# Kernel optimization log

Measured on AMD Instinct MI355X. Metric: run time of the kernel, lower is better.

Reference implementation:

```python
import math
import jax, jax.numpy as jnp
import numpy as np

B, S, D, H = 2, 2048, 1024, 16
DK = D // H


def alibi_slopes(n_heads):
    # canonical ALiBi slopes for power-of-two head counts: 2^(-8*(h+1)/H)
    ratio = 2.0 ** (-8.0 / n_heads)
    return jnp.asarray(ratio ** np.arange(1, n_heads + 1), dtype=jnp.float32)


def setup_inputs() -> dict:
    key = jax.random.key(0)
    ks = jax.random.split(key, 8)
    std = 1.0 / math.sqrt(D)
    return {
        "query": jax.random.normal(ks[0], (B, S, D), jnp.float32),
        "key": jax.random.normal(ks[1], (B, S, D), jnp.float32),
        "value": jax.random.normal(ks[2], (B, S, D), jnp.float32),
        "mask": jnp.ones((B, S, S), jnp.int32),
        "Wq": jax.random.normal(ks[3], (D, D), jnp.float32) * std,
        "bq": jnp.zeros((D,), jnp.float32),
        "Wk": jax.random.normal(ks[4], (D, D), jnp.float32) * std,
        "bk": jnp.zeros((D,), jnp.float32),
        "Wv": jax.random.normal(ks[5], (D, D), jnp.float32) * std,
        "bv": jnp.zeros((D,), jnp.float32),
        "Wo": jax.random.normal(ks[6], (D, D), jnp.float32) * std,
        "bo": jnp.zeros((D,), jnp.float32),
    }


def _split_heads(x):
    # [B, S, D] -> [B, H, S, DK]
    return x.reshape(B, -1, H, DK).transpose(0, 2, 1, 3)


def reference(query, key, value, mask, Wq, bq, Wk, bk, Wv, bv, Wo, bo):
    q = _split_heads(query @ Wq + bq)
    k = _split_heads(key @ Wk + bk)
    v = _split_heads(value @ Wv + bv)
    scores = jnp.einsum("bhqd,bhkd->bhqk", q, k) / math.sqrt(DK)
    # ALiBi bias: -slope_h * |i - j|, shape [H, S, S]
    pos = jnp.arange(S)
    dist = jnp.abs(pos[:, None] - pos[None, :]).astype(jnp.float32)
    bias = -alibi_slopes(H)[:, None, None] * dist
    scores = scores + bias[None]
    scores = jnp.where(mask[:, None] == 0, -jnp.inf, scores)
    p_attn = jax.nn.softmax(scores, axis=-1)
    out = jnp.einsum("bhqk,bhkd->bhqd", p_attn, v)
    out = out.transpose(0, 2, 1, 3).reshape(B, -1, D)
    return out @ Wo + bo
```

## Files before the change

kernel.cpp:

```cpp
#include <hip/hip_runtime.h>
#include <hip/hip_bf16.h>
#include <math.h>

constexpr int Bb  = 2;
constexpr int Ss  = 2048;
constexpr int Dd  = 1024;
constexpr int Hh  = 16;
constexpr int DKk = 64;
constexpr int Mm  = Bb * Ss;

#define QSCALE 0.18033688f

typedef unsigned short u16;
typedef unsigned int   u32;
typedef __attribute__((ext_vector_type(8))) short short8;
typedef __attribute__((ext_vector_type(4))) short short4v;
typedef __attribute__((ext_vector_type(4))) float f32x4;
typedef __attribute__((ext_vector_type(4))) int   int4v;

static __device__ __forceinline__ u16 f2bf(float f) {
  union { float f; unsigned u; } c; c.f = f;
  unsigned u = c.u;
  unsigned r = u + 0x7FFFu + ((u >> 16) & 1u);
  return (u16)(r >> 16);
}

static __device__ __forceinline__ void gl_lds16(const u16* g, u16* l) {
  __builtin_amdgcn_global_load_lds(
      (const __attribute__((address_space(1))) u32*)g,
      (__attribute__((address_space(3))) u32*)l, 16, 0, 0);
}

__global__ __launch_bounds__(256) void cvt_inputs(
    const float* __restrict__ q, const float* __restrict__ k,
    const float* __restrict__ v, u16* __restrict__ outA)
{
  const size_t per = (size_t)Mm * Dd / 4;
  const size_t tot = 3 * per;
  for (size_t i = (size_t)blockIdx.x * blockDim.x + threadIdx.x; i < tot;
       i += (size_t)gridDim.x * blockDim.x) {
    const float* src; size_t idx;
    if (i < per)            { src = q; idx = i; }
    else if (i < 2 * per)   { src = k; idx = i - per; }
    else                    { src = v; idx = i - 2 * per; }
    f32x4 f = ((const f32x4*)src)[idx];
    short4v o;
    o[0] = (short)f2bf(f[0]); o[1] = (short)f2bf(f[1]);
    o[2] = (short)f2bf(f[2]); o[3] = (short)f2bf(f[3]);
    ((short4v*)outA)[i] = o;
  }
}

__global__ __launch_bounds__(256) void wt_transpose(
    const float* __restrict__ wq, const float* __restrict__ wk,
    const float* __restrict__ wv, const float* __restrict__ wo,
    u16* __restrict__ outWT)
{
  __shared__ float tile[64][65];
  const int z = blockIdx.z;
  const float* w = (z == 0) ? wq : (z == 1) ? wk : (z == 2) ? wv : wo;
  const int n0 = blockIdx.x * 64, k0 = blockIdx.y * 64;
  const int t = threadIdx.x;
  {
    const int r = t >> 2, u = t & 3;
    #pragma unroll
    for (int e = 0; e < 4; e++) {
      f32x4 f = *(const f32x4*)(w + (size_t)(k0 + r) * Dd + n0 + u * 16 + e * 4);
      tile[r][u * 16 + e * 4 + 0] = f[0];
      tile[r][u * 16 + e * 4 + 1] = f[1];
      tile[r][u * 16 + e * 4 + 2] = f[2];
      tile[r][u * 16 + e * 4 + 3] = f[3];
    }
  }
  __syncthreads();
  {
    const int n = t >> 2, u = t & 3;
    u16 tmp[16];
    #pragma unroll
    for (int e = 0; e < 16; e++) tmp[e] = f2bf(tile[u * 16 + e][n]);
    short8 o0, o1;
    #pragma unroll
    for (int j = 0; j < 8; j++) { o0[j] = (short)tmp[j]; o1[j] = (short)tmp[8 + j]; }
    u16* dst = outWT + (size_t)z * Dd * Dd + (size_t)(n0 + n) * Dd + k0 + u * 16;
    *(short8*)dst       = o0;
    *(short8*)(dst + 8) = o1;
  }
}

__global__ __launch_bounds__(256) void mask_flags(
    const int* __restrict__ mask, int* __restrict__ flags)
{
  const int fid = blockIdx.x;
  const int b = fid >> 10, qt = (fid >> 5) & 31, kt = fid & 31;
  const int t = threadIdx.x;
  int hasz = 0;
  #pragma unroll
  for (int e = 0; e < 4; e++) {
    int c = t + 256 * e;
    int row = c >> 4, c4 = c & 15;
    int4v mv = *(const int4v*)(mask + ((size_t)b * Ss + qt * 64 + row) * Ss + kt * 64 + c4 * 4);
    hasz |= (mv[0] == 0) | (mv[1] == 0) | (mv[2] == 0) | (mv[3] == 0);
  }
  __shared__ int red;
  if (t == 0) red = 0;
  __syncthreads();
  if (hasz) atomicOr(&red, 1);
  __syncthreads();
  if (t == 0) flags[fid] = red;
}

__global__ __launch_bounds__(256, 4) void gemm_qkv(
    const u16* __restrict__ Aall, const u16* __restrict__ WT,
    const float* __restrict__ bq, const float* __restrict__ bk,
    const float* __restrict__ bv,
    u16* __restrict__ Qh, u16* __restrict__ Kh, u16* __restrict__ Vt)
{
  const int bid   = blockIdx.x;
  const int swzid = (bid & 7) * 96 + (bid >> 3);
  const int z     = swzid >> 8;
  const int rem   = swzid & 255;
  const int mbase = (rem >> 3) * 128, nbase = (rem & 7) * 128;

  const u16* A  = Aall + (size_t)z * Mm * Dd;
  const u16* Bw = WT   + (size_t)z * Dd * Dd;
  const float* bias = (z == 0) ? bq : (z == 1) ? bk : bv;

  __shared__ u16 lA[2][128][32];
  __shared__ u16 lB[2][128][32];

  const int t = threadIdx.x, lane = t & 63, w = t >> 6;
  const int wr = w >> 1, wc = w & 1, lg = lane >> 4, lr = lane & 15;
  const int srow = lane >> 2;
  const int scol = (lane & 3) * 8;

  f32x4 acc[4][4];
  #pragma unroll
  for (int mf = 0; mf < 4; mf++)
    #pragma unroll
    for (int nf = 0; nf < 4; nf++) acc[mf][nf] = (f32x4){0.f, 0.f, 0.f, 0.f};

  const u16* ga0 = A  + (size_t)(mbase + w * 16       + srow) * Dd + scol;
  const u16* ga1 = A  + (size_t)(mbase + (w + 4) * 16 + srow) * Dd + scol;
  const u16* gb0 = Bw + (size_t)(nbase + w * 16       + srow) * Dd + scol;
  const u16* gb1 = Bw + (size_t)(nbase + (w + 4) * 16 + srow) * Dd + scol;

  #define GSTAGE(buf, kk_)                              \
    {                                                   \
      gl_lds16(ga0 + (kk_), &lA[buf][w * 16][0]);       \
      gl_lds16(ga1 + (kk_), &lA[buf][(w + 4) * 16][0]); \
      gl_lds16(gb0 + (kk_), &lB[buf][w * 16][0]);       \
      gl_lds16(gb1 + (kk_), &lB[buf][(w + 4) * 16][0]); \
    }

  GSTAGE(0, 0);
  __syncthreads();
  int cur = 0;

  for (int kk = 0; kk < Dd; kk += 32) {
    if (kk + 32 < Dd) GSTAGE(cur ^ 1, kk + 32);
    short8 af[4], bfr[4];
    #pragma unroll
    for (int mf = 0; mf < 4; mf++) af[mf]  = *(const short8*)&lA[cur][wr * 64 + mf * 16 + lr][lg * 8];
    #pragma unroll
    for (int nf = 0; nf < 4; nf++) bfr[nf] = *(const short8*)&lB[cur][wc * 64 + nf * 16 + lr][lg * 8];
    __builtin_amdgcn_s_setprio(1);
    #pragma unroll
    for (int mf = 0; mf < 4; mf++)
      #pragma unroll
      for (int nf = 0; nf < 4; nf++)
        acc[mf][nf] = __builtin_amdgcn_mfma_f32_16x16x32_bf16(af[mf], bfr[nf], acc[mf][nf], 0, 0, 0);
    __builtin_amdgcn_s_setprio(0);
    __syncthreads();
    cur ^= 1;
  }
  #undef GSTAGE

  #pragma unroll
  for (int nf = 0; nf < 4; nf++) {
    const int n = nbase + wc * 64 + nf * 16 + lr;
    const float bb = bias[n];
    const int h = n >> 6, dk = n & 63;
    #pragma unroll
    for (int mf = 0; mf < 4; mf++) {
      const int m0 = mbase + wr * 64 + mf * 16 + lg * 4;
      const int b = m0 >> 11, s0 = m0 & 2047;
      if (z == 2) {
        short4v o;
        #pragma unroll
        for (int r = 0; r < 4; r++) o[r] = (short)f2bf(acc[mf][nf][r] + bb);
        *(short4v*)(Vt + ((size_t)(b * Hh + h) * DKk + dk) * Ss + s0) = o;
      } else if (z == 0) {
        #pragma unroll
        for (int r = 0; r < 4; r++)
          Qh[((size_t)(b * Hh + h) * Ss + s0 + r) * DKk + dk] =
              f2bf((acc[mf][nf][r] + bb) * QSCALE);
      } else {
        #pragma unroll
        for (int r = 0; r < 4; r++)
          Kh[((size_t)(b * Hh + h) * Ss + s0 + r) * DKk + dk] = f2bf(acc[mf][nf][r] + bb);
      }
    }
  }
}

__global__ __launch_bounds__(256, 4) void attn_kernel(
    const u16* __restrict__ Qh, const u16* __restrict__ Kh, const u16* __restrict__ Vt,
    const int* __restrict__ mask, const int* __restrict__ flags,
    float* __restrict__ Pacc, float* __restrict__ Sacc, u16* __restrict__ AO)
{
  const int bid = blockIdx.x;
  const int t = threadIdx.x, lane = t & 63, w = t >> 6;
  const int lg = lane >> 4, lr = lane & 15;

  __shared__ u16 lK[2][64][64];
  __shared__ u16 lV[2][64][64];
  __shared__ u16 lP[4][16][64];

  const int swz  = lr & 7;
  const int sxor = (lr & 7) << 4;
  char* lpb = (char*)&lP[w][0][0];

  const int srr = lane >> 3;
  const int scs = ((lane & 7) ^ srr) * 8;

  short8 ones;
  #pragma unroll
  for (int j = 0; j < 8; j++) ones[j] = (short)0x3F80;

  const int nit = (bid >= 512) ? 2 : 1;

  for (int it = 0; it < nit; ++it) {
    int b, h, qt, p, split;
    if (it == 0) {
      h = 15 - (bid >> 7);
      const int rem = bid & 127;
      b = rem >> 6; qt = (rem >> 1) & 31; p = rem & 1; split = 1;
    } else {
      const int sidx = bid - 512, group = sidx >> 7, within = sidx & 127;
      h = group * 2 + (within >> 6);
      b = (within >> 5) & 1; qt = within & 31; p = 0; split = 0;
    }

    const u16* Qp = Qh + ((size_t)(b * Hh + h) * Ss + qt * 64 + w * 16) * DKk;
    const u16* Kp = Kh + ((size_t)(b * Hh + h) * Ss) * DKk;
    const u16* Vp = Vt + ((size_t)(b * Hh + h) * DKk) * Ss;

    const short8 qf0 = *(const short8*)(Qp + lr * DKk + lg * 8);
    const short8 qf1 = *(const short8*)(Qp + lr * DKk + 32 + lg * 8);

    const float slope_n = exp2f(-0.5f * (float)(h + 1));
    const float slope2  = slope_n * 1.44269504f;
    const float binc    = 64.0f * slope2;

    const int W = (int)(__builtin_fmaf(0.3466f, (float)(h + 1), 14.0f) / slope_n);
    const int q0 = qt * 64;
    int kt0 = max(0, (q0 - W) >> 6);
    int kt1 = min((int)(Ss / 64) - 1, (q0 + 63 + W) >> 6);
    if (split) { const int mid = (kt0 + kt1 + 1) >> 1; if (p == 0) kt1 = mid - 1; else kt0 = mid; }

    f32x4 accO[4], acc5;
    #pragma unroll
    for (int nf = 0; nf < 4; nf++) accO[nf] = (f32x4){0.f, 0.f, 0.f, 0.f};
    acc5 = (f32x4){0.f, 0.f, 0.f, 0.f};

    const int   qg  = qt * 64 + w * 16 + lr;
    const float qgf = (float)qg;
    const int flg_base = (b * 32 + qt) * 32;
    f32x4 bias[4];

    #define STAGE(buf, kt_)                                                          \
      {                                                                              \
        _Pragma("unroll")                                                            \
        for (int j = 0; j < 2; j++) {                                                \
          const int row = w * 16 + j * 8 + srr;                                      \
          gl_lds16(Kp + (size_t)((kt_) * 64 + row) * DKk + scs, &lK[buf][w * 16 + j * 8][0]); \
          gl_lds16(Vp + (size_t)row * Ss + (kt_) * 64 + scs,    &lV[buf][w * 16 + j * 8][0]); \
        }                                                                            \
      }

    STAGE(0, kt0);
    __syncthreads();
    int cur = 0;

    for (int kt = kt0; kt <= kt1; kt++) {
      if (kt < kt1) STAGE(cur ^ 1, kt + 1);

      if (kt == kt0 || kt == qt || kt == qt + 1) {
        #pragma unroll
        for (int kf = 0; kf < 4; kf++) {
          const float dif = qgf - (float)(kt * 64 + kf * 16 + lg * 4);
          #pragma unroll
          for (int r = 0; r < 4; r++)
            bias[kf][r] = -slope2 * __builtin_fabsf(dif - (float)r);
        }
      } else {
        const float step = (kt < qt) ? binc : -binc;
        #pragma unroll
        for (int kf = 0; kf < 4; kf++)
          #pragma unroll
          for (int r = 0; r < 4; r++) bias[kf][r] += step;
      }

      f32x4 ex[4];
      __builtin_amdgcn_s_setprio(1);
      #pragma unroll
      for (int kf = 0; kf < 4; kf++) {
        const short8 kb0 = *(const short8*)&lK[cur][kf * 16 + lr][((lg)     ^ swz) * 8];
        const short8 kb1 = *(const short8*)&lK[cur][kf * 16 + lr][((lg + 4) ^ swz) * 8];
        f32x4 z = __builtin_amdgcn_mfma_f32_16x16x32_bf16(kb0, qf0, bias[kf], 0, 0, 0);
        ex[kf]  = __builtin_amdgcn_mfma_f32_16x16x32_bf16(kb1, qf1, z, 0, 0, 0);
      }
      __builtin_amdgcn_s_setprio(0);

      const int flagv = flags[flg_base + kt];
      if (flagv) {
        #pragma unroll
        for (int kf = 0; kf < 4; kf++)
          #pragma unroll
          for (int r = 0; r < 4; r++) {
            const int key = kt * 64 + kf * 16 + lg * 4 + r;
            if (mask[((size_t)b * Ss + qg) * Ss + key] == 0) ex[kf][r] = -3.0e38f;
          }
      }

      #pragma unroll
      for (int kf = 0; kf < 4; kf++) {
        short4v pkv;
        #pragma unroll
        for (int r = 0; r < 4; r++) {
          const float pv = exp2f(ex[kf][r]);
          pkv[r] = (short)(u16)((__float_as_uint(pv) + 0x8000u) >> 16);
        }
        *(short4v*)(lpb + lr * 128 + ((kf * 32 + lg * 8) ^ sxor)) = pkv;
      }

      asm volatile("s_waitcnt lgkmcnt(0)" ::: "memory");
      __builtin_amdgcn_sched_barrier(0);

      const short8 pf0 = *(const short8*)(lpb + lr * 128 + ((lg * 16) ^ sxor));
      const short8 pf1 = *(const short8*)(lpb + lr * 128 + ((64 + lg * 16) ^ sxor));
      __builtin_amdgcn_s_setprio(1);
      #pragma unroll
      for (int nf = 0; nf < 4; nf++) {
        const short8 va0 = *(const short8*)&lV[cur][nf * 16 + lr][((lg)     ^ swz) * 8];
        const short8 va1 = *(const short8*)&lV[cur][nf * 16 + lr][((lg + 4) ^ swz) * 8];
        accO[nf] = __builtin_amdgcn_mfma_f32_16x16x32_bf16(va0, pf0, accO[nf], 0, 0, 0);
        accO[nf] = __builtin_amdgcn_mfma_f32_16x16x32_bf16(va1, pf1, accO[nf], 0, 0, 0);
      }
      acc5 = __builtin_amdgcn_mfma_f32_16x16x32_bf16(ones, pf0, acc5, 0, 0, 0);
      acc5 = __builtin_amdgcn_mfma_f32_16x16x32_bf16(ones, pf1, acc5, 0, 0, 0);
      __builtin_amdgcn_s_setprio(0);

      __syncthreads();
      cur ^= 1;
    }
    #undef STAGE

    if (!split) {
      const float rinv = 1.0f / acc5[0];
      u16* aop = AO + (size_t)(b * Ss + qt * 64 + w * 16 + lr) * Dd + h * DKk;
      #pragma unroll
      for (int nf = 0; nf < 4; nf++) {
        short4v ov;
        #pragma unroll
        for (int r = 0; r < 4; r++) ov[r] = (short)f2bf(accO[nf][r] * rinv);
        *(short4v*)(aop + nf * 16 + lg * 4) = ov;
      }
    } else {
      const size_t rowid = (((size_t)p * 2 + b) * 8 + (h - 8)) * Ss + qt * 64 + w * 16 + lr;
      float* pb = Pacc + rowid * DKk;
      #pragma unroll
      for (int nf = 0; nf < 4; nf++)
        *(f32x4*)(pb + nf * 16 + lg * 4) = accO[nf];
      if (lg == 0) Sacc[rowid] = acc5[0];
    }
  }
}

__global__ __launch_bounds__(256) void attn_norm(
    const float* __restrict__ Pacc, const float* __restrict__ Sacc,
    u16* __restrict__ AO)
{
  const int R  = blockIdx.x * 16 + (threadIdx.x >> 4);
  const int dq = (threadIdx.x & 15) * 4;
  const float l = Sacc[R] + Sacc[32768 + R];
  const float rinv = 1.0f / l;
  const f32x4 a = *(const f32x4*)(Pacc + (size_t)R * 64 + dq);
  const f32x4 c = *(const f32x4*)(Pacc + (size_t)32768 * 64 + (size_t)R * 64 + dq);
  short4v o;
  #pragma unroll
  for (int r = 0; r < 4; r++) o[r] = (short)f2bf((a[r] + c[r]) * rinv);
  const int s = R & 2047, h8 = (R >> 11) & 7, b = R >> 14;
  *(short4v*)(AO + ((size_t)b * Ss + s) * Dd + (h8 + 8) * 64 + dq) = o;
}

__global__ __launch_bounds__(256, 4) void gemm_out(
    const u16* __restrict__ A, const u16* __restrict__ Bw,
    const float* __restrict__ bo, float* __restrict__ out)
{
  const int bid   = blockIdx.x;
  const int swzid = (bid & 7) * 32 + (bid >> 3);
  const int mbase = (swzid >> 3) * 128, nbase = (swzid & 7) * 128;

  __shared__ u16 lA[2][128][32];
  __shared__ u16 lB[2][128][32];
  const int t = threadIdx.x, lane = t & 63, w = t >> 6;
  const int wr = w >> 1, wc = w & 1, lg = lane >> 4, lr = lane & 15;
  const int srow = lane >> 2, scol = (lane & 3) * 8;

  f32x4 acc[4][4];
  #pragma unroll
  for (int mf = 0; mf < 4; mf++)
    #pragma unroll
    for (int nf = 0; nf < 4; nf++) acc[mf][nf] = (f32x4){0.f, 0.f, 0.f, 0.f};

  const u16* ga0 = A  + (size_t)(mbase + w * 16       + srow) * Dd + scol;
  const u16* ga1 = A  + (size_t)(mbase + (w + 4) * 16 + srow) * Dd + scol;
  const u16* gb0 = Bw + (size_t)(nbase + w * 16       + srow) * Dd + scol;
  const u16* gb1 = Bw + (size_t)(nbase + (w + 4) * 16 + srow) * Dd + scol;

  #define GSTAGE(buf, kk_)                              \
    {                                                   \
      gl_lds16(ga0 + (kk_), &lA[buf][w * 16][0]);       \
      gl_lds16(ga1 + (kk_), &lA[buf][(w + 4) * 16][0]); \
      gl_lds16(gb0 + (kk_), &lB[buf][w * 16][0]);       \
      gl_lds16(gb1 + (kk_), &lB[buf][(w + 4) * 16][0]); \
    }

  GSTAGE(0, 0);
  __syncthreads();
  int cur = 0;

  for (int kk = 0; kk < Dd; kk += 32) {
    if (kk + 32 < Dd) GSTAGE(cur ^ 1, kk + 32);
    short8 af[4], bfr[4];
    #pragma unroll
    for (int mf = 0; mf < 4; mf++) af[mf]  = *(const short8*)&lA[cur][wr * 64 + mf * 16 + lr][lg * 8];
    #pragma unroll
    for (int nf = 0; nf < 4; nf++) bfr[nf] = *(const short8*)&lB[cur][wc * 64 + nf * 16 + lr][lg * 8];
    __builtin_amdgcn_s_setprio(1);
    #pragma unroll
    for (int mf = 0; mf < 4; mf++)
      #pragma unroll
      for (int nf = 0; nf < 4; nf++)
        acc[mf][nf] = __builtin_amdgcn_mfma_f32_16x16x32_bf16(af[mf], bfr[nf], acc[mf][nf], 0, 0, 0);
    __builtin_amdgcn_s_setprio(0);
    __syncthreads();
    cur ^= 1;
  }
  #undef GSTAGE

  #pragma unroll
  for (int nf = 0; nf < 4; nf++) {
    const int n = nbase + wc * 64 + nf * 16 + lr;
    const float bb = bo[n];
    #pragma unroll
    for (int mf = 0; mf < 4; mf++) {
      const int m0 = mbase + wr * 64 + mf * 16 + lg * 4;
      #pragma unroll
      for (int r = 0; r < 4; r++)
        out[(size_t)(m0 + r) * Dd + n] = acc[mf][nf][r] + bb;
    }
  }
}

extern "C" void kernel_launch(void* const* d_in, const int* in_sizes, int n_in,
                              void* d_out, int out_size, void* d_ws, size_t ws_size,
                              hipStream_t stream)
{
  (void)in_sizes; (void)n_in; (void)out_size; (void)ws_size;
  const float* q    = (const float*)d_in[0];
  const float* k    = (const float*)d_in[1];
  const float* v    = (const float*)d_in[2];
  const int*   mask = (const int*)  d_in[3];
  const float* Wq   = (const float*)d_in[4];
  const float* bq   = (const float*)d_in[5];
  const float* Wk   = (const float*)d_in[6];
  const float* bk   = (const float*)d_in[7];
  const float* Wv   = (const float*)d_in[8];
  const float* bv   = (const float*)d_in[9];
  const float* Wo   = (const float*)d_in[10];
  const float* bo   = (const float*)d_in[11];

  char* ws = (char*)d_ws;
  u16* A_bf  = (u16*)(ws + 0);
  u16* WT    = (u16*)(ws + 25165824);
  u16* Qh    = (u16*)(ws + 33554432);
  u16* Kh    = (u16*)(ws + 41943040);
  u16* Vt    = (u16*)(ws + 50331648);
  u16* AO    = (u16*)(ws + 58720256);
  int* flags = (int*)(ws + 67108864);
  float* Pacc = (float*)(ws + 0);
  float* Sacc = (float*)(ws + 16777216);

  cvt_inputs  <<<2048, 256, 0, stream>>>(q, k, v, A_bf);
  wt_transpose<<<dim3(16, 16, 4), 256, 0, stream>>>(Wq, Wk, Wv, Wo, WT);
  mask_flags  <<<2048, 256, 0, stream>>>(mask, flags);
  gemm_qkv    <<<768, 256, 0, stream>>>(A_bf, WT, bq, bk, bv, Qh, Kh, Vt);
  attn_kernel <<<1024, 256, 0, stream>>>(Qh, Kh, Vt, mask, flags, Pacc, Sacc, AO);
  attn_norm   <<<2048, 256, 0, stream>>>(Pacc, Sacc, AO);
  gemm_out    <<<256, 256, 0, stream>>>(AO, WT + (size_t)3 * Dd * Dd, bo, (float*)d_out);
}
```

Baseline: 132.6 us.

## Fuse fp32-to-bf16 input conversion into QKV GEMM and merge prep kernels

Drops the separate cvt_inputs pass. The QKV GEMM now stages fp32 activation tiles straight into LDS with a swizzled layout and converts them to bf16 in registers before the MFMA. The weight transpose and mask-flag kernels are merged into one launch. This removes a full write and re-read of the bf16 activation copy and two kernel launches, at the cost of twice the LDS for the A tile and lower occupancy (launch bounds 4 to 3).

```diff
diff --git a/kernel.cpp b/kernel.cpp
--- a/kernel.cpp
+++ b/kernel.cpp
@@ -25,92 +25,78 @@
   return (u16)(r >> 16);
 }
 
-static __device__ __forceinline__ void gl_lds16(const u16* g, u16* l) {
+static __device__ __forceinline__ u32 pk2(float a, float b) {
+  __hip_bfloat162 t = __float22bfloat162_rn(float2{a, b});
+  union { __hip_bfloat162 h; u32 u; } c; c.h = t;
+  return c.u;
+}
+
+static __device__ __forceinline__ void gl_lds16(const void* g, void* l) {
   __builtin_amdgcn_global_load_lds(
       (const __attribute__((address_space(1))) u32*)g,
       (__attribute__((address_space(3))) u32*)l, 16, 0, 0);
 }
 
-__global__ __launch_bounds__(256) void cvt_inputs(
-    const float* __restrict__ q, const float* __restrict__ k,
-    const float* __restrict__ v, u16* __restrict__ outA)
-{
-  const size_t per = (size_t)Mm * Dd / 4;
-  const size_t tot = 3 * per;
-  for (size_t i = (size_t)blockIdx.x * blockDim.x + threadIdx.x; i < tot;
-       i += (size_t)gridDim.x * blockDim.x) {
-    const float* src; size_t idx;
-    if (i < per)            { src = q; idx = i; }
-    else if (i < 2 * per)   { src = k; idx = i - per; }
-    else                    { src = v; idx = i - 2 * per; }
-    f32x4 f = ((const f32x4*)src)[idx];
-    short4v o;
-    o[0] = (short)f2bf(f[0]); o[1] = (short)f2bf(f[1]);
-    o[2] = (short)f2bf(f[2]); o[3] = (short)f2bf(f[3]);
-    ((short4v*)outA)[i] = o;
-  }
-}
-
-__global__ __launch_bounds__(256) void wt_transpose(
+__global__ __launch_bounds__(256) void prep(
     const float* __restrict__ wq, const float* __restrict__ wk,
     const float* __restrict__ wv, const float* __restrict__ wo,
-    u16* __restrict__ outWT)
-{
-  __shared__ float tile[64][65];
-  const int z = blockIdx.z;
-  const float* w = (z == 0) ? wq : (z == 1) ? wk : (z == 2) ? wv : wo;
-  const int n0 = blockIdx.x * 64, k0 = blockIdx.y * 64;
-  const int t = threadIdx.x;
-  {
-    const int r = t >> 2, u = t & 3;
-    #pragma unroll
-    for (int e = 0; e < 4; e++) {
-      f32x4 f = *(const f32x4*)(w + (size_t)(k0 + r) * Dd + n0 + u * 16 + e * 4);
-      tile[r][u * 16 + e * 4 + 0] = f[0];
-      tile[r][u * 16 + e * 4 + 1] = f[1];
-      tile[r][u * 16 + e * 4 + 2] = f[2];
-      tile[r][u * 16 + e * 4 + 3] = f[3];
-    }
-  }
-  __syncthreads();
-  {
-    const int n = t >> 2, u = t & 3;
-    u16 tmp[16];
-    #pragma unroll
-    for (int e = 0; e < 16; e++) tmp[e] = f2bf(tile[u * 16 + e][n]);
-    short8 o0, o1;
-    #pragma unroll
-    for (int j = 0; j < 8; j++) { o0[j] = (short)tmp[j]; o1[j] = (short)tmp[8 + j]; }
-    u16* dst = outWT + (size_t)z * Dd * Dd + (size_t)(n0 + n) * Dd + k0 + u * 16;
-    *(short8*)dst       = o0;
-    *(short8*)(dst + 8) = o1;
-  }
-}
-
-__global__ __launch_bounds__(256) void mask_flags(
+    u16* __restrict__ outWT,
     const int* __restrict__ mask, int* __restrict__ flags)
 {
-  const int fid = blockIdx.x;
-  const int b = fid >> 10, qt = (fid >> 5) & 31, kt = fid & 31;
+  const int bid = blockIdx.x;
   const int t = threadIdx.x;
-  int hasz = 0;
-  #pragma unroll
-  for (int e = 0; e < 4; e++) {
-    int c = t + 256 * e;
-    int row = c >> 4, c4 = c & 15;
-    int4v mv = *(const int4v*)(mask + ((size_t)b * Ss + qt * 64 + row) * Ss + kt * 64 + c4 * 4);
-    hasz |= (mv[0] == 0) | (mv[1] == 0) | (mv[2] == 0) | (mv[3] == 0);
+  if (bid < 1024) {
+    __shared__ float tile[64][65];
+    const int z = bid >> 8;
+    const float* w = (z == 0) ? wq : (z == 1) ? wk : (z == 2) ? wv : wo;
+    const int n0 = (bid & 15) * 64, k0 = ((bid >> 4) & 15) * 64;
+    {
+      const int r = t >> 2, u = t & 3;
+      #pragma unroll
+      for (int e = 0; e < 4; e++) {
+        f32x4 f = *(const f32x4*)(w + (size_t)(k0 + r) * Dd + n0 + u * 16 + e * 4);
+        tile[r][u * 16 + e * 4 + 0] = f[0];
+        tile[r][u * 16 + e * 4 + 1] = f[1];
+        tile[r][u * 16 + e * 4 + 2] = f[2];
+        tile[r][u * 16 + e * 4 + 3] = f[3];
+      }
+    }
+    __syncthreads();
+    {
+      const int n = t >> 2, u = t & 3;
+      u16 tmp[16];
+      #pragma unroll
+      for (int e = 0; e < 16; e++) tmp[e] = f2bf(tile[u * 16 + e][n]);
+      short8 o0, o1;
+      #pragma unroll
+      for (int j = 0; j < 8; j++) { o0[j] = (short)tmp[j]; o1[j] = (short)tmp[8 + j]; }
+      u16* dst = outWT + (size_t)z * Dd * Dd + (size_t)(n0 + n) * Dd + k0 + u * 16;
+      *(short8*)dst       = o0;
+      *(short8*)(dst + 8) = o1;
+    }
+  } else {
+    const int fid = bid - 1024;
+    const int b = fid >> 10, qt = (fid >> 5) & 31, kt = fid & 31;
+    int hasz = 0;
+    #pragma unroll
+    for (int e = 0; e < 4; e++) {
+      int c = t + 256 * e;
+      int row = c >> 4, c4 = c & 15;
+      int4v mv = *(const int4v*)(mask + ((size_t)b * Ss + qt * 64 + row) * Ss + kt * 64 + c4 * 4);
+      hasz |= (mv[0] == 0) | (mv[1] == 0) | (mv[2] == 0) | (mv[3] == 0);
+    }
+    __shared__ int red;
+    if (t == 0) red = 0;
+    __syncthreads();
+    if (hasz) atomicOr(&red, 1);
+    __syncthreads();
+    if (t == 0) flags[fid] = red;
   }
-  __shared__ int red;
-  if (t == 0) red = 0;
-  __syncthreads();
-  if (hasz) atomicOr(&red, 1);
-  __syncthreads();
-  if (t == 0) flags[fid] = red;
-}
-
-__global__ __launch_bounds__(256, 4) void gemm_qkv(
-    const u16* __restrict__ Aall, const u16* __restrict__ WT,
+}
+
+__global__ __launch_bounds__(256, 3) void gemm_qkv(
+    const float* __restrict__ qin, const float* __restrict__ kin,
+    const float* __restrict__ vin, const u16* __restrict__ WT,
     const float* __restrict__ bq, const float* __restrict__ bk,
     const float* __restrict__ bv,
     u16* __restrict__ Qh, u16* __restrict__ Kh, u16* __restrict__ Vt)
@@ -121,35 +107,42 @@
   const int rem   = swzid & 255;
   const int mbase = (rem >> 3) * 128, nbase = (rem & 7) * 128;
 
-  const u16* A  = Aall + (size_t)z * Mm * Dd;
-  const u16* Bw = WT   + (size_t)z * Dd * Dd;
+  const float* Af = (z == 0) ? qin : (z == 1) ? kin : vin;
+  const u16*   Bw = WT + (size_t)z * Dd * Dd;
   const float* bias = (z == 0) ? bq : (z == 1) ? bk : bv;
 
-  __shared__ u16 lA[2][128][32];
-  __shared__ u16 lB[2][128][32];
+  __shared__ float lAf[2][128][32];
+  __shared__ u16   lB[2][128][32];
 
   const int t = threadIdx.x, lane = t & 63, w = t >> 6;
   const int wr = w >> 1, wc = w & 1, lg = lane >> 4, lr = lane & 15;
   const int srow = lane >> 2;
   const int scol = (lane & 3) * 8;
 
+  const int arow8 = lane >> 3;
+  const int ascs  = ((lane & 7) ^ arow8) * 4;
+  const int aswz  = lr & 7;
+  const int aoff0 = (((2 * lg)     ^ aswz) * 4);
+  const int aoff1 = (((2 * lg + 1) ^ aswz) * 4);
+
   f32x4 acc[4][4];
   #pragma unroll
   for (int mf = 0; mf < 4; mf++)
     #pragma unroll
     for (int nf = 0; nf < 4; nf++) acc[mf][nf] = (f32x4){0.f, 0.f, 0.f, 0.f};
 
-  const u16* ga0 = A  + (size_t)(mbase + w * 16       + srow) * Dd + scol;
-  const u16* ga1 = A  + (size_t)(mbase + (w + 4) * 16 + srow) * Dd + scol;
   const u16* gb0 = Bw + (size_t)(nbase + w * 16       + srow) * Dd + scol;
   const u16* gb1 = Bw + (size_t)(nbase + (w + 4) * 16 + srow) * Dd + scol;
 
-  #define GSTAGE(buf, kk_)                              \
-    {                                                   \
-      gl_lds16(ga0 + (kk_), &lA[buf][w * 16][0]);       \
-      gl_lds16(ga1 + (kk_), &lA[buf][(w + 4) * 16][0]); \
-      gl_lds16(gb0 + (kk_), &lB[buf][w * 16][0]);       \
-      gl_lds16(gb1 + (kk_), &lB[buf][(w + 4) * 16][0]); \
+  #define GSTAGE(buf, kk_)                                                        \
+    {                                                                             \
+      _Pragma("unroll")                                                           \
+      for (int j = 0; j < 4; j++) {                                               \
+        const int row = mbase + j * 32 + w * 8 + arow8;                           \
+        gl_lds16(Af + (size_t)row * Dd + (kk_) + ascs, &lAf[buf][j * 32 + w * 8][0]); \
+      }                                                                           \
+      gl_lds16(gb0 + (kk_), &lB[buf][w * 16][0]);                                 \
+      gl_lds16(gb1 + (kk_), &lB[buf][(w + 4) * 16][0]);                           \
     }
 
   GSTAGE(0, 0);
@@ -158,9 +151,20 @@
 
   for (int kk = 0; kk < Dd; kk += 32) {
     if (kk + 32 < Dd) GSTAGE(cur ^ 1, kk + 32);
-    short8 af[4], bfr[4];
-    #pragma unroll
-    for (int mf = 0; mf < 4; mf++) af[mf]  = *(const short8*)&lA[cur][wr * 64 + mf * 16 + lr][lg * 8];
+    short8 af[4];
+    #pragma unroll
+    for (int mf = 0; mf < 4; mf++) {
+      const float* arow = &lAf[cur][wr * 64 + mf * 16 + lr][0];
+      const f32x4 c0 = *(const f32x4*)(arow + aoff0);
+      const f32x4 c1 = *(const f32x4*)(arow + aoff1);
+      int4v pv;
+      pv[0] = (int)pk2(c0[0], c0[1]);
+      pv[1] = (int)pk2(c0[2], c0[3]);
+      pv[2] = (int)pk2(c1[0], c1[1]);
+      pv[3] = (int)pk2(c1[2], c1[3]);
+      af[mf] = *(short8*)&pv;
+    }
+    short8 bfr[4];
     #pragma unroll
     for (int nf = 0; nf < 4; nf++) bfr[nf] = *(const short8*)&lB[cur][wc * 64 + nf * 16 + lr][lg * 8];
     __builtin_amdgcn_s_setprio(1);
@@ -483,7 +487,6 @@
   const float* bo   = (const float*)d_in[11];
 
   char* ws = (char*)d_ws;
-  u16* A_bf  = (u16*)(ws + 0);
   u16* WT    = (u16*)(ws + 25165824);
   u16* Qh    = (u16*)(ws + 33554432);
   u16* Kh    = (u16*)(ws + 41943040);
@@ -493,10 +496,8 @@
   float* Pacc = (float*)(ws + 0);
   float* Sacc = (float*)(ws + 16777216);
 
-  cvt_inputs  <<<2048, 256, 0, stream>>>(q, k, v, A_bf);
-  wt_transpose<<<dim3(16, 16, 4), 256, 0, stream>>>(Wq, Wk, Wv, Wo, WT);
-  mask_flags  <<<2048, 256, 0, stream>>>(mask, flags);
-  gemm_qkv    <<<768, 256, 0, stream>>>(A_bf, WT, bq, bk, bv, Qh, Kh, Vt);
+  prep        <<<3072, 256, 0, stream>>>(Wq, Wk, Wv, Wo, WT, mask, flags);
+  gemm_qkv    <<<768, 256, 0, stream>>>(q, k, v, WT, bq, bk, bv, Qh, Kh, Vt);
   attn_kernel <<<1024, 256, 0, stream>>>(Qh, Kh, Vt, mask, flags, Pacc, Sacc, AO);
   attn_norm   <<<2048, 256, 0, stream>>>(Pacc, Sacc, AO);
   gemm_out    <<<256, 256, 0, stream>>>(AO, WT + (size_t)3 * Dd * Dd, bo, (float*)d_out);
```

After: 126.6 us. 4.5% less time.
